# Performance work log

Hardware: AMD Instinct MI355X
Metric: run time of the kernel (lower is better)

The kernel has to match this reference:

```python
import jax, jax.numpy as jnp
import numpy as np

IN_SIZE = 448
OUT_SIZE = 224


def _sig10(z):
    return jax.nn.sigmoid(10.0 * z)


def _crop_resize_one(img, loc):
    # img: [3, H, W] float32, loc: [3] = (tx, ty, tl) in pixel units
    in_size = img.shape[1]
    tx, ty, tl = loc[0], loc[1], loc[2]
    # clamp tl exactly as torch code does (in_size == 448 branch)
    if in_size == 448:
        tl = jnp.maximum(tl, in_size / 3.0)
    else:
        tl = jnp.clip(tl, in_size / 4.0, in_size * 3.0 / 8.0)
    tx = jnp.clip(tx, tl, in_size - tl)
    ty = jnp.clip(ty, tl, in_size - tl)
    # int() truncation on nonnegative values == floor
    w_off = jnp.maximum(jnp.floor(tx - tl), 0.0)
    h_off = jnp.maximum(jnp.floor(ty - tl), 0.0)
    w_end = jnp.minimum(jnp.floor(tx + tl), float(in_size))
    h_end = jnp.minimum(jnp.floor(ty + tl), float(in_size))

    # sigmoid soft mask over the full image: rows ~ w axis, cols ~ h axis
    idx = jnp.arange(in_size, dtype=jnp.float32)
    mrow = _sig10(idx - w_off) - _sig10(idx - w_end)   # [H]
    mcol = _sig10(idx - h_off) - _sig10(idx - h_end)   # [W]
    xatt = img * (mrow[:, None] * mcol[None, :])        # [3, H, W]

    # fused crop + bilinear resize to OUT_SIZE, align_corners=True:
    # src coordinate = off + j * (crop_len - 1) / (OUT_SIZE - 1)
    j = jnp.arange(OUT_SIZE, dtype=jnp.float32)
    src_r = w_off + j * (w_end - w_off - 1.0) / (OUT_SIZE - 1)  # [224]
    src_c = h_off + j * (h_end - h_off - 1.0) / (OUT_SIZE - 1)  # [224]

    r0 = jnp.clip(jnp.floor(src_r), 0.0, in_size - 1.0)
    c0 = jnp.clip(jnp.floor(src_c), 0.0, in_size - 1.0)
    wr = src_r - r0  # fractional weights
    wc = src_c - c0
    r0i = r0.astype(jnp.int32)
    c0i = c0.astype(jnp.int32)
    r1i = jnp.minimum(r0i + 1, in_size - 1)
    c1i = jnp.minimum(c0i + 1, in_size - 1)

    top = xatt[:, r0i, :]      # [3, 224, W]
    bot = xatt[:, r1i, :]      # [3, 224, W]
    x00 = top[:, :, c0i]       # [3, 224, 224]
    x01 = top[:, :, c1i]
    x10 = bot[:, :, c0i]
    x11 = bot[:, :, c1i]

    wr_ = wr[None, :, None]
    wc_ = wc[None, None, :]
    return (1.0 - wr_) * ((1.0 - wc_) * x00 + wc_ * x01) + wr_ * ((1.0 - wc_) * x10 + wc_ * x11)


def setup_inputs() -> dict:
    key = jax.random.key(0)
    k1, k2 = jax.random.split(key)
    B = 64
    images = jax.random.normal(k1, (B, 3, IN_SIZE, IN_SIZE), dtype=jnp.float32)
    # locs = sigmoid(apn) * [1,1,0.5] * in_size  ->  tx,ty in (0,448), tl in (0,224)
    scale = jnp.array([IN_SIZE, IN_SIZE, IN_SIZE // 2], dtype=jnp.float32)
    locs = jax.random.uniform(k2, (B, 3), dtype=jnp.float32) * scale
    return {"images": images, "locs": locs}


def reference(images, locs):
    # AttentionCropLayer forward: per-sample soft-mask crop + bilinear resize,
    # vectorized over the batch instead of the original Python loop.
    return jax.vmap(_crop_resize_one)(images, locs)  # [B, 3, 224, 224]
```

## Files before the change

### kernel.cpp

```cpp
#include <hip/hip_runtime.h>
#include <cmath>

#define IN_SZ  448
#define OUT_SZ 224
#define RPB    8

__device__ __forceinline__ float sig10(float z) {
    return 1.0f / (1.0f + expf(-10.0f * z));
}

__global__ __launch_bounds__(256) void racnn_kernel(
    const float* __restrict__ img,
    const float* __restrict__ locs,
    float* __restrict__ out)
{
    const int b   = blockIdx.y;
    const int rg  = blockIdx.x;
    const int tid = threadIdx.x;

    __shared__ int   s_r0[RPB], s_r1[RPB];
    __shared__ float s_a0[RPB], s_a1[RPB];

    float tx = locs[b * 3 + 0];
    float ty = locs[b * 3 + 1];
    float tl = locs[b * 3 + 2];
    tl = fmaxf(tl, (float)IN_SZ / 3.0f);
    tx = fminf(fmaxf(tx, tl), (float)IN_SZ - tl);
    ty = fminf(fmaxf(ty, tl), (float)IN_SZ - tl);
    const float w_off = fmaxf(floorf(tx - tl), 0.0f);
    const float h_off = fmaxf(floorf(ty - tl), 0.0f);
    const float w_end = fminf(floorf(tx + tl), (float)IN_SZ);
    const float h_end = fminf(floorf(ty + tl), (float)IN_SZ);

    if (tid < RPB) {
        int jr = rg * RPB + tid;
        float src_r = w_off + (float)jr * (w_end - w_off - 1.0f) / (float)(OUT_SZ - 1);
        float r0 = fminf(fmaxf(floorf(src_r), 0.0f), (float)(IN_SZ - 1));
        float wr = src_r - r0;
        int r0i = (int)r0;
        int r1i = min(r0i + 1, IN_SZ - 1);
        float m0 = sig10(r0 - w_off) - sig10(r0 - w_end);
        float m1 = sig10((float)r1i - w_off) - sig10((float)r1i - w_end);
        s_r0[tid] = r0i;
        s_r1[tid] = r1i;
        s_a0[tid] = (1.0f - wr) * m0;
        s_a1[tid] = wr * m1;
    }

    int   c0i = 0, c1i = 0;
    float b0 = 0.0f, b1 = 0.0f;
    if (tid < OUT_SZ) {
        float src_c = h_off + (float)tid * (h_end - h_off - 1.0f) / (float)(OUT_SZ - 1);
        float c0 = fminf(fmaxf(floorf(src_c), 0.0f), (float)(IN_SZ - 1));
        float wc = src_c - c0;
        c0i = (int)c0;
        c1i = min(c0i + 1, IN_SZ - 1);
        float m0 = sig10(c0 - h_off) - sig10(c0 - h_end);
        float m1 = sig10((float)c1i - h_off) - sig10((float)c1i - h_end);
        b0 = (1.0f - wc) * m0;
        b1 = wc * m1;
    }

    __syncthreads();
    if (tid >= OUT_SZ) return;

    const size_t img_b = (size_t)b * 3 * IN_SZ * IN_SZ;
    const size_t out_b = (size_t)b * 3 * OUT_SZ * OUT_SZ;

    #pragma unroll
    for (int ch = 0; ch < 3; ++ch) {
        const float* cbase = img + img_b + (size_t)ch * IN_SZ * IN_SZ;
        float* obase = out + out_b + (size_t)ch * OUT_SZ * OUT_SZ
                     + (size_t)(rg * RPB) * OUT_SZ + tid;
        #pragma unroll
        for (int k = 0; k < RPB; ++k) {
            const float* row0 = cbase + s_r0[k] * IN_SZ;
            const float* row1 = cbase + s_r1[k] * IN_SZ;
            float x00 = row0[c0i];
            float x01 = row0[c1i];
            float x10 = row1[c0i];
            float x11 = row1[c1i];
            float v = s_a0[k] * (b0 * x00 + b1 * x01)
                    + s_a1[k] * (b0 * x10 + b1 * x11);
            obase[(size_t)k * OUT_SZ] = v;
        }
    }
}

extern "C" void kernel_launch(void* const* d_in, const int* in_sizes, int n_in,
                              void* d_out, int out_size, void* d_ws, size_t ws_size,
                              hipStream_t stream) {
    const float* img  = (const float*)d_in[0];
    const float* locs = (const float*)d_in[1];
    float* out = (float*)d_out;
    const int B = in_sizes[1] / 3;
    dim3 grid(OUT_SZ / RPB, B);
    racnn_kernel<<<grid, 256, 0, stream>>>(img, locs, out);
}
```

Baseline: 228.1 us.

## Stage needed input rows in shared memory with float4 loads before bilinear gather

Each block now copies the band of source rows it needs for one channel (up to 18 rows, restricted to the used column range) into LDS with coalesced float4 loads, then does the bilinear gather from LDS instead of scattered global loads. This targets uncoalesced, redundant global reads in the gather. In exchange it adds about 32KB of LDS per block and two barriers per channel, which may lower occupancy and serialize load and compute. It assumes the row span never exceeds 18 rows.

After: 223.5 us. 2.0% less time.

```diff
diff --git a/kernel.cpp b/kernel.cpp
--- a/kernel.cpp
+++ b/kernel.cpp
@@ -1,9 +1,11 @@
 #include <hip/hip_runtime.h>
 #include <cmath>
 
-#define IN_SZ  448
-#define OUT_SZ 224
-#define RPB    8
+#define IN_SZ   448
+#define OUT_SZ  224
+#define RPB     8
+#define NROWS   18
+#define ROWF4   (IN_SZ / 4)
 
 __device__ __forceinline__ float sig10(float z) {
     return 1.0f / (1.0f + expf(-10.0f * z));
@@ -18,6 +20,7 @@
     const int rg  = blockIdx.x;
     const int tid = threadIdx.x;
 
+    __shared__ float s_img[NROWS * IN_SZ];
     __shared__ int   s_r0[RPB], s_r1[RPB];
     __shared__ float s_a0[RPB], s_a1[RPB];
 
@@ -32,9 +35,12 @@
     const float w_end = fminf(floorf(tx + tl), (float)IN_SZ);
     const float h_end = fminf(floorf(ty + tl), (float)IN_SZ);
 
+    const float rstep = (w_end - w_off - 1.0f) / (float)(OUT_SZ - 1);
+    const float cstep = (h_end - h_off - 1.0f) / (float)(OUT_SZ - 1);
+
     if (tid < RPB) {
         int jr = rg * RPB + tid;
-        float src_r = w_off + (float)jr * (w_end - w_off - 1.0f) / (float)(OUT_SZ - 1);
+        float src_r = w_off + (float)jr * rstep;
         float r0 = fminf(fmaxf(floorf(src_r), 0.0f), (float)(IN_SZ - 1));
         float wr = src_r - r0;
         int r0i = (int)r0;
@@ -47,42 +53,61 @@
         s_a1[tid] = wr * m1;
     }
 
-    int   c0i = 0, c1i = 0;
-    float b0 = 0.0f, b1 = 0.0f;
-    if (tid < OUT_SZ) {
-        float src_c = h_off + (float)tid * (h_end - h_off - 1.0f) / (float)(OUT_SZ - 1);
+    int   c0i, c1i;
+    float cb0, cb1;
+    {
+        float src_c = h_off + (float)min(tid, OUT_SZ - 1) * cstep;
         float c0 = fminf(fmaxf(floorf(src_c), 0.0f), (float)(IN_SZ - 1));
         float wc = src_c - c0;
         c0i = (int)c0;
         c1i = min(c0i + 1, IN_SZ - 1);
         float m0 = sig10(c0 - h_off) - sig10(c0 - h_end);
         float m1 = sig10((float)c1i - h_off) - sig10((float)c1i - h_end);
-        b0 = (1.0f - wc) * m0;
-        b1 = wc * m1;
+        cb0 = (1.0f - wc) * m0;
+        cb1 = wc * m1;
     }
 
-    __syncthreads();
-    if (tid >= OUT_SZ) return;
+    int row_lo  = (int)fminf(fmaxf(floorf(w_off + (float)(rg * RPB) * rstep), 0.0f), (float)(IN_SZ - 1));
+    int r0_last = (int)fminf(fmaxf(floorf(w_off + (float)(rg * RPB + RPB - 1) * rstep), 0.0f), (float)(IN_SZ - 1));
+    int row_hi  = min(r0_last + 1, IN_SZ - 1);
+    int nrows   = row_hi - row_lo + 1;
+
+    int c_lo  = (int)fminf(fmaxf(floorf(h_off), 0.0f), (float)(IN_SZ - 1));
+    int chl   = (int)fminf(fmaxf(floorf(h_off + (float)(OUT_SZ - 1) * cstep), 0.0f), (float)(IN_SZ - 1));
+    int c_hi  = min(chl + 1, IN_SZ - 1);
+    int c4base = c_lo >> 2;
+    int nf4    = (c_hi >> 2) - c4base + 1;
 
     const size_t img_b = (size_t)b * 3 * IN_SZ * IN_SZ;
     const size_t out_b = (size_t)b * 3 * OUT_SZ * OUT_SZ;
 
-    #pragma unroll
+    const int lr = tid >> 7;
+    const int lc = tid & 127;
+
     for (int ch = 0; ch < 3; ++ch) {
-        const float* cbase = img + img_b + (size_t)ch * IN_SZ * IN_SZ;
-        float* obase = out + out_b + (size_t)ch * OUT_SZ * OUT_SZ
-                     + (size_t)(rg * RPB) * OUT_SZ + tid;
+        __syncthreads();
+        const float4* src4 = (const float4*)(img + img_b + (size_t)ch * IN_SZ * IN_SZ);
+        float4* dst4 = (float4*)s_img;
         #pragma unroll
-        for (int k = 0; k < RPB; ++k) {
-            const float* row0 = cbase + s_r0[k] * IN_SZ;
-            const float* row1 = cbase + s_r1[k] * IN_SZ;
-            float x00 = row0[c0i];
-            float x01 = row0[c1i];
-            float x10 = row1[c0i];
-            float x11 = row1[c1i];
-            float v = s_a0[k] * (b0 * x00 + b1 * x01)
-                    + s_a1[k] * (b0 * x10 + b1 * x11);
-            obase[(size_t)k * OUT_SZ] = v;
+        for (int rr = 0; rr < NROWS; rr += 2) {
+            int r = rr + lr;
+            if (r < nrows && lc < nf4) {
+                dst4[r * ROWF4 + c4base + lc] = src4[(size_t)(row_lo + r) * ROWF4 + c4base + lc];
+            }
+        }
+        __syncthreads();
+        if (tid < OUT_SZ) {
+            float* obase = out + out_b + (size_t)ch * OUT_SZ * OUT_SZ
+                         + (size_t)(rg * RPB) * OUT_SZ + tid;
+            #pragma unroll
+            for (int k = 0; k < RPB; ++k) {
+                const float* p0 = s_img + (s_r0[k] - row_lo) * IN_SZ;
+                const float* p1 = s_img + (s_r1[k] - row_lo) * IN_SZ;
+                float x00 = p0[c0i], x01 = p0[c1i];
+                float x10 = p1[c0i], x11 = p1[c1i];
+                obase[(size_t)k * OUT_SZ] =
+                    s_a0[k] * (cb0 * x00 + cb1 * x01) + s_a1[k] * (cb0 * x10 + cb1 * x11);
+            }
         }
     }
 }
```
